# Optimization experiments

Hardware: AMD Instinct MI355X
Metric: run time of the kernel (lower is better)

## Reference

```python
import jax, jax.numpy as jnp
import numpy as np

K = 3   # kernel_size
D = 1   # dilation
G = 8   # groups
BN_EPS = 1e-5


def setup_inputs() -> dict:
    key = jax.random.key(0)
    ks = jax.random.split(key, 8)
    N, C, H, W = 8, 64, 256, 256
    k2 = K * K
    x = jax.random.normal(ks[0], (N, C, H, W), jnp.float32)
    conv_w = jax.random.normal(ks[1], (G * k2, C), jnp.float32) * (2.0 / C) ** 0.5
    bn_gamma = jnp.ones((G * k2,), jnp.float32)
    bn_beta = jnp.zeros((G * k2,), jnp.float32)
    bn_mean = jax.random.normal(ks[2], (G * k2,), jnp.float32) * 0.01
    bn_var = jax.random.uniform(ks[3], (G * k2,), jnp.float32, 0.5, 1.5)
    lamb_l = jax.random.normal(ks[4], (C,), jnp.float32) * 0.1
    lamb_h = jax.random.normal(ks[5], (C,), jnp.float32) * 0.1
    inside_all = jax.random.normal(ks[6], (C, 1, 1), jnp.float32) * 0.1
    return {"x": x, "conv_w": conv_w, "bn_gamma": bn_gamma, "bn_beta": bn_beta,
            "bn_mean": bn_mean, "bn_var": bn_var, "lamb_l": lamb_l,
            "lamb_h": lamb_h, "inside_all": inside_all}


def reference(x, conv_w, bn_gamma, bn_beta, bn_mean, bn_var, lamb_l, lamb_h, inside_all):
    N, C, H, W = x.shape
    k2 = K * K
    # ap: adaptive avg pool to (1,1) -> (N, C)
    pooled = x.mean(axis=(2, 3))
    # 1x1 conv on a 1x1 map == matmul; then eval-mode BatchNorm
    lf = pooled @ conv_w.T                                   # (N, G*k2)
    lf = (lf - bn_mean) * (bn_gamma / jnp.sqrt(bn_var + BN_EPS)) + bn_beta
    lf = jnp.tanh(lf).reshape(N, G, 1, k2, 1)                # (N, G, 1, k2, 1)
    # im2col/unfold with reflection padding; ordering matches torch (C, kh, kw)
    p = D * (K - 1) // 2
    xp = jnp.pad(x, ((0, 0), (0, 0), (p, p), (p, p)), mode="reflect")
    patches = jnp.stack(
        [xp[:, :, i * D:i * D + H, j * D:j * D + W] for i in range(K) for j in range(K)],
        axis=2,
    )                                                        # (N, C, k2, H, W)
    xu = patches.reshape(N, G, C // G, k2, H * W)
    low_part = jnp.sum(xu * lf, axis=3).reshape(N, C, H, W)  # per-pixel dynamic filter
    # DSA: gap pools to (1,1)
    gap = x.mean(axis=(2, 3), keepdims=True)                 # (N, C, 1, 1)
    out_low = (low_part * (inside_all + 1.0) - inside_all * gap) * lamb_l[None, :, None, None]
    out_high = x * (lamb_h[None, :, None, None] + 1.0)
    return out_low + out_high
```

## Files before the change

kernel.cpp:

```cpp
#include <hip/hip_runtime.h>
#include <math.h>

#define NN 8
#define CC 64
#define HH 256
#define WW 256
#define GG 8
#define K2 9
#define OC 72
#define BN_EPS 1e-5f

__global__ __launch_bounds__(256) void pool_kernel(const float* __restrict__ x,
                                                   float* __restrict__ pooled) {
    int nc = blockIdx.x;
    const float4* p4 = (const float4*)(x + (size_t)nc * (HH * WW));
    float s = 0.f;
    for (int i = threadIdx.x; i < (HH * WW) / 4; i += 256) {
        float4 v = p4[i];
        s += (v.x + v.y) + (v.z + v.w);
    }
    for (int off = 32; off > 0; off >>= 1) s += __shfl_down(s, off, 64);
    __shared__ float smem[4];
    int lane = threadIdx.x & 63, wid = threadIdx.x >> 6;
    if (lane == 0) smem[wid] = s;
    __syncthreads();
    if (threadIdx.x == 0) {
        float t = (smem[0] + smem[1]) + (smem[2] + smem[3]);
        pooled[nc] = t * (1.0f / (HH * WW));
    }
}

__global__ __launch_bounds__(256) void lf_kernel(const float* __restrict__ pooled,
                                                 const float* __restrict__ conv_w,
                                                 const float* __restrict__ gamma,
                                                 const float* __restrict__ beta,
                                                 const float* __restrict__ mean,
                                                 const float* __restrict__ var,
                                                 float* __restrict__ lf) {
    int j = blockIdx.x * blockDim.x + threadIdx.x;
    if (j >= NN * OC) return;
    int n = j / OC, oc = j % OC;
    const float* pw = conv_w + oc * CC;
    const float* pp = pooled + n * CC;
    float acc = 0.f;
#pragma unroll 8
    for (int c = 0; c < CC; ++c) acc += pp[c] * pw[c];
    float inv = gamma[oc] / sqrtf(var[oc] + BN_EPS);
    lf[j] = tanhf((acc - mean[oc]) * inv + beta[oc]);
}

__global__ __launch_bounds__(256) void main_kernel(const float* __restrict__ x,
                                                   const float* __restrict__ lf,
                                                   const float* __restrict__ pooled,
                                                   const float* __restrict__ lamb_l,
                                                   const float* __restrict__ lamb_h,
                                                   const float* __restrict__ ia,
                                                   float* __restrict__ out) {
    const int wid  = threadIdx.x >> 6;
    const int lane = threadIdx.x & 63;
    const int nc     = blockIdx.x >> 6;
    const int h      = ((blockIdx.x & 63) << 2) + wid;
    const int c      = nc & (CC - 1);
    const int n      = nc >> 6;
    const int g      = c >> 3;

    const float* lw = lf + (n * OC + g * K2);
    const float w00 = lw[0], w01 = lw[1], w02 = lw[2];
    const float w10 = lw[3], w11 = lw[4], w12 = lw[5];
    const float w20 = lw[6], w21 = lw[7], w22 = lw[8];
    const float ll    = lamb_l[c];
    const float lh1   = lamb_h[c] + 1.0f;
    const float iav   = ia[c];
    const float scale = iav + 1.0f;
    const float bias  = -iav * pooled[nc];

    const float* base = x + (size_t)nc * (HH * WW);
    const int hm = (h == 0) ? 1 : h - 1;
    const int hp = (h == HH - 1) ? HH - 2 : h + 1;
    const float4 vt = ((const float4*)(base + hm * WW))[lane];
    const float4 vm = ((const float4*)(base + (size_t)h * WW))[lane];
    const float4 vb = ((const float4*)(base + hp * WW))[lane];

    float lt = __shfl_up(vt.w, 1, 64);   if (lane == 0)  lt = vt.y;
    float lm = __shfl_up(vm.w, 1, 64);   if (lane == 0)  lm = vm.y;
    float lb = __shfl_up(vb.w, 1, 64);   if (lane == 0)  lb = vb.y;
    float rt = __shfl_down(vt.x, 1, 64); if (lane == 63) rt = vt.z;
    float rm = __shfl_down(vm.x, 1, 64); if (lane == 63) rm = vm.z;
    float rb = __shfl_down(vb.x, 1, 64); if (lane == 63) rb = vb.z;

    const float t[6] = {lt, vt.x, vt.y, vt.z, vt.w, rt};
    const float m[6] = {lm, vm.x, vm.y, vm.z, vm.w, rm};
    const float b[6] = {lb, vb.x, vb.y, vb.z, vb.w, rb};

    float4 o;
    float* op = &o.x;
#pragma unroll
    for (int k = 0; k < 4; ++k) {
        float acc = w00 * t[k] + w01 * t[k + 1] + w02 * t[k + 2]
                  + w10 * m[k] + w11 * m[k + 1] + w12 * m[k + 2]
                  + w20 * b[k] + w21 * b[k + 1] + w22 * b[k + 2];
        op[k] = ll * (scale * acc + bias) + lh1 * m[k + 1];
    }
    ((float4*)(out + (size_t)nc * (HH * WW) + (size_t)h * WW))[lane] = o;
}

extern "C" void kernel_launch(void* const* d_in, const int* in_sizes, int n_in,
                              void* d_out, int out_size, void* d_ws, size_t ws_size,
                              hipStream_t stream) {
    const float* x      = (const float*)d_in[0];
    const float* conv_w = (const float*)d_in[1];
    const float* gamma  = (const float*)d_in[2];
    const float* beta   = (const float*)d_in[3];
    const float* mean   = (const float*)d_in[4];
    const float* var    = (const float*)d_in[5];
    const float* lamb_l = (const float*)d_in[6];
    const float* lamb_h = (const float*)d_in[7];
    const float* ia     = (const float*)d_in[8];
    float* out = (float*)d_out;

    float* pooled = (float*)d_ws;
    float* lf     = pooled + NN * CC;

    pool_kernel<<<NN * CC, 256, 0, stream>>>(x, pooled);
    lf_kernel<<<(NN * OC + 255) / 256, 256, 0, stream>>>(pooled, conv_w, gamma, beta,
                                                         mean, var, lf);
    main_kernel<<<NN * CC * (HH / 4), 256, 0, stream>>>(x, lf, pooled, lamb_l, lamb_h,
                                                        ia, out);
}
```

Measured before the change: 279.1 us.

## Compute four rows per wave with shared halo rows; widen pool blocks

```diff
diff --git a/kernel.cpp b/kernel.cpp
--- a/kernel.cpp
+++ b/kernel.cpp
@@ -10,23 +10,25 @@
 #define OC 72
 #define BN_EPS 1e-5f
 
-__global__ __launch_bounds__(256) void pool_kernel(const float* __restrict__ x,
-                                                   float* __restrict__ pooled) {
+__global__ __launch_bounds__(1024) void pool_kernel(const float* __restrict__ x,
+                                                    float* __restrict__ pooled) {
     int nc = blockIdx.x;
     const float4* p4 = (const float4*)(x + (size_t)nc * (HH * WW));
     float s = 0.f;
-    for (int i = threadIdx.x; i < (HH * WW) / 4; i += 256) {
+#pragma unroll 4
+    for (int i = threadIdx.x; i < (HH * WW) / 4; i += 1024) {
         float4 v = p4[i];
         s += (v.x + v.y) + (v.z + v.w);
     }
     for (int off = 32; off > 0; off >>= 1) s += __shfl_down(s, off, 64);
-    __shared__ float smem[4];
+    __shared__ float smem[16];
     int lane = threadIdx.x & 63, wid = threadIdx.x >> 6;
     if (lane == 0) smem[wid] = s;
     __syncthreads();
-    if (threadIdx.x == 0) {
-        float t = (smem[0] + smem[1]) + (smem[2] + smem[3]);
-        pooled[nc] = t * (1.0f / (HH * WW));
+    if (threadIdx.x < 16) {
+        float t = smem[threadIdx.x];
+        for (int off = 8; off > 0; off >>= 1) t += __shfl_down(t, off, 64);
+        if (threadIdx.x == 0) pooled[nc] = t * (1.0f / (HH * WW));
     }
 }
 
@@ -58,11 +60,11 @@
                                                    float* __restrict__ out) {
     const int wid  = threadIdx.x >> 6;
     const int lane = threadIdx.x & 63;
-    const int nc     = blockIdx.x >> 6;
-    const int h      = ((blockIdx.x & 63) << 2) + wid;
-    const int c      = nc & (CC - 1);
-    const int n      = nc >> 6;
-    const int g      = c >> 3;
+    const int nc   = blockIdx.x >> 4;
+    const int r0   = ((blockIdx.x & 15) << 4) + (wid << 2);
+    const int c    = nc & (CC - 1);
+    const int n    = nc >> 6;
+    const int g    = c >> 3;
 
     const float* lw = lf + (n * OC + g * K2);
     const float w00 = lw[0], w01 = lw[1], w02 = lw[2];
@@ -75,33 +77,38 @@
     const float bias  = -iav * pooled[nc];
 
     const float* base = x + (size_t)nc * (HH * WW);
-    const int hm = (h == 0) ? 1 : h - 1;
-    const int hp = (h == HH - 1) ? HH - 2 : h + 1;
-    const float4 vt = ((const float4*)(base + hm * WW))[lane];
-    const float4 vm = ((const float4*)(base + (size_t)h * WW))[lane];
-    const float4 vb = ((const float4*)(base + hp * WW))[lane];
 
-    float lt = __shfl_up(vt.w, 1, 64);   if (lane == 0)  lt = vt.y;
-    float lm = __shfl_up(vm.w, 1, 64);   if (lane == 0)  lm = vm.y;
-    float lb = __shfl_up(vb.w, 1, 64);   if (lane == 0)  lb = vb.y;
-    float rt = __shfl_down(vt.x, 1, 64); if (lane == 63) rt = vt.z;
-    float rm = __shfl_down(vm.x, 1, 64); if (lane == 63) rm = vm.z;
-    float rb = __shfl_down(vb.x, 1, 64); if (lane == 63) rb = vb.z;
+    float4 v[6];
+    float  L[6], R[6];
+#pragma unroll
+    for (int i = 0; i < 6; ++i) {
+        int r = r0 - 1 + i;
+        r = (r < 0) ? 1 : ((r > HH - 1) ? HH - 2 : r);
+        v[i] = ((const float4*)(base + r * WW))[lane];
+    }
+#pragma unroll
+    for (int i = 0; i < 6; ++i) {
+        L[i] = __shfl_up(v[i].w, 1, 64);   if (lane == 0)  L[i] = v[i].y;
+        R[i] = __shfl_down(v[i].x, 1, 64); if (lane == 63) R[i] = v[i].z;
+    }
 
-    const float t[6] = {lt, vt.x, vt.y, vt.z, vt.w, rt};
-    const float m[6] = {lm, vm.x, vm.y, vm.z, vm.w, rm};
-    const float b[6] = {lb, vb.x, vb.y, vb.z, vb.w, rb};
-
-    float4 o;
-    float* op = &o.x;
+    float* outbase = out + (size_t)nc * (HH * WW);
 #pragma unroll
-    for (int k = 0; k < 4; ++k) {
-        float acc = w00 * t[k] + w01 * t[k + 1] + w02 * t[k + 2]
-                  + w10 * m[k] + w11 * m[k + 1] + w12 * m[k + 2]
-                  + w20 * b[k] + w21 * b[k + 1] + w22 * b[k + 2];
-        op[k] = ll * (scale * acc + bias) + lh1 * m[k + 1];
+    for (int j = 0; j < 4; ++j) {
+        const float t[6] = {L[j],   v[j].x,   v[j].y,   v[j].z,   v[j].w,   R[j]};
+        const float m[6] = {L[j+1], v[j+1].x, v[j+1].y, v[j+1].z, v[j+1].w, R[j+1]};
+        const float b[6] = {L[j+2], v[j+2].x, v[j+2].y, v[j+2].z, v[j+2].w, R[j+2]};
+        float4 o;
+        float* op = &o.x;
+#pragma unroll
+        for (int k = 0; k < 4; ++k) {
+            float acc = w00 * t[k] + w01 * t[k + 1] + w02 * t[k + 2]
+                      + w10 * m[k] + w11 * m[k + 1] + w12 * m[k + 2]
+                      + w20 * b[k] + w21 * b[k + 1] + w22 * b[k + 2];
+            op[k] = ll * (scale * acc + bias) + lh1 * m[k + 1];
+        }
+        ((float4*)(outbase + (size_t)(r0 + j) * WW))[lane] = o;
     }
-    ((float4*)(out + (size_t)nc * (HH * WW) + (size_t)h * WW))[lane] = o;
 }
 
 extern "C" void kernel_launch(void* const* d_in, const int* in_sizes, int n_in,
@@ -121,9 +128,9 @@
     float* pooled = (float*)d_ws;
     float* lf     = pooled + NN * CC;
 
-    pool_kernel<<<NN * CC, 256, 0, stream>>>(x, pooled);
+    pool_kernel<<<NN * CC, 1024, 0, stream>>>(x, pooled);
     lf_kernel<<<(NN * OC + 255) / 256, 256, 0, stream>>>(pooled, conv_w, gamma, beta,
                                                          mean, var, lf);
-    main_kernel<<<NN * CC * (HH / 4), 256, 0, stream>>>(x, lf, pooled, lamb_l, lamb_h,
-                                                        ia, out);
+    main_kernel<<<NN * CC * (HH / 16), 256, 0, stream>>>(x, lf, pooled, lamb_l, lamb_h,
+                                                         ia, out);
 }
```

Result: faster. 266.5 us (-4.5%).
